# Performance work log

Hardware: AMD Instinct MI355X
Metric: run time of the kernel (lower is better)

The kernel has to match this reference:

```python
import jax, jax.numpy as jnp
import numpy as np

DIM = 1024
STATE = 256
B, S = 4, 4096

def setup_inputs() -> dict:
    key = jax.random.key(0)
    ks = jax.random.split(key, 8)
    sc_b = 1.0 / np.sqrt(DIM)
    sc_c = 1.0 / np.sqrt(STATE)
    return {
        "x": jax.random.normal(ks[0], (B, S, DIM), dtype=jnp.float32),
        "A": jax.random.normal(ks[1], (STATE,), dtype=jnp.float32) * 0.02,
        "B_w": jax.random.uniform(ks[2], (STATE, DIM), minval=-sc_b, maxval=sc_b),
        "B_b": jax.random.uniform(ks[3], (STATE,), minval=-sc_b, maxval=sc_b),
        "C_w": jax.random.uniform(ks[4], (DIM, STATE), minval=-sc_c, maxval=sc_c),
        "C_b": jax.random.uniform(ks[5], (DIM,), minval=-sc_c, maxval=sc_c),
        "D_w": jax.random.uniform(ks[6], (DIM, DIM), minval=-sc_b, maxval=sc_b),
        "D_b": jax.random.uniform(ks[7], (DIM,), minval=-sc_b, maxval=sc_b),
    }

def reference(x, A, B_w, B_b, C_w, C_b, D_w, D_b):
    # Precompute input projections in batch (the per-step loop only needs state*A + Bu)
    Bu = jnp.einsum('bsd,nd->bsn', x, B_w) + B_b          # [B,S,STATE]
    Du = jnp.einsum('bsd,ed->bse', x, D_w) + D_b          # [B,S,DIM]
    Aexp = jnp.exp(A)[None, :]                             # [1,STATE]
    state0 = jnp.zeros((x.shape[0], A.shape[0]), dtype=x.dtype)

    def step(state, bu_t):
        state = jnp.tanh(state * Aexp + bu_t)
        return state, state

    _, states = jax.lax.scan(step, state0, jnp.swapaxes(Bu, 0, 1))  # [S,B,STATE]
    states = jnp.swapaxes(states, 0, 1)                              # [B,S,STATE]
    y = jnp.einsum('bsn,en->bse', states, C_w) + C_b + Du
    return y
```

## Files before the change

### kernel.cpp

```cpp
#include <hip/hip_runtime.h>
#include <hip/hip_bf16.h>

#define DIM 1024
#define STATE 256
#define BATCH 4
#define SEQ 4096
#define M_TOT (BATCH * SEQ)

typedef short short8 __attribute__((ext_vector_type(8)));
typedef float f32x4 __attribute__((ext_vector_type(4)));

__device__ __forceinline__ unsigned short f2bf(float f) {
  unsigned int u = __float_as_uint(f);
  u += 0x7fff + ((u >> 16) & 1);
  return (unsigned short)(u >> 16);
}

__device__ __forceinline__ void gl_lds16(const void* g, void* l) {
  __builtin_amdgcn_global_load_lds(
      (const __attribute__((address_space(1))) void*)g,
      (__attribute__((address_space(3))) void*)l, 16, 0, 0);
}

#define C2F 2.8853900817779268f
#define LOG2EF 1.4426950408889634f
#define VMC(N) asm volatile("s_waitcnt vmcnt(" #N ")" ::: "memory")

__global__ __launch_bounds__(256) void convert_w(
    const float* __restrict__ A, const float* __restrict__ Bw,
    const float* __restrict__ Bb, const float* __restrict__ Cw,
    const float* __restrict__ Cb, const float* __restrict__ Dw,
    const float* __restrict__ Db, unsigned short* __restrict__ bwb,
    unsigned short* __restrict__ wob, float* __restrict__ bb2,
    float* __restrict__ mP2, float* __restrict__ cbdb) {
  const int bx = blockIdx.x;
  const int t = threadIdx.x;
  if (bx < 256) {
    int c = t * 4;
    const float4 v = *(const float4*)(Bw + (size_t)bx * DIM + c);
    *(ushort4*)(bwb + (size_t)bx * DIM + c) =
        make_ushort4(f2bf(v.x), f2bf(v.y), f2bf(v.z), f2bf(v.w));
  } else if (bx < 256 + 1024) {
    int e = bx - 256;
    if (t < 64) {
      const float4 v = *(const float4*)(Cw + (size_t)e * STATE + t * 4);
      *(ushort4*)(wob + (size_t)e * 1280 + t * 4) =
          make_ushort4(f2bf(v.x), f2bf(v.y), f2bf(v.z), f2bf(v.w));
    }
    const float4 v = *(const float4*)(Dw + (size_t)e * DIM + t * 4);
    *(ushort4*)(wob + (size_t)e * 1280 + 256 + t * 4) =
        make_ushort4(f2bf(v.x), f2bf(v.y), f2bf(v.z), f2bf(v.w));
  } else {
    const float P = C2F * __builtin_amdgcn_exp2f(A[t] * LOG2EF);
    bb2[t] = fmaf(Bb[t], C2F, P);
    mP2[t] = -2.0f * P;
#pragma unroll
    for (int k = 0; k < 4; ++k) {
      const int i = t * 4 + k;
      cbdb[i] = Cb[i] + Db[i];
    }
  }
}

__global__ __launch_bounds__(256, 2) void gemm_GX(
    const float* __restrict__ x,
    const unsigned short* __restrict__ bwb,
    float* __restrict__ G,
    const float* __restrict__ bb2,
    unsigned short* __restrict__ xb)
{
  __shared__ char lds[61440];

  const int tid = threadIdx.x;
  const int wave = tid >> 6;
  const int lane = tid & 63;
  const int lr = lane & 15;
  const int lk = lane >> 4;
  const int m0 = blockIdx.x * 32;

  f32x4 acc[2][4];
#pragma unroll
  for (int i = 0; i < 2; ++i)
#pragma unroll
    for (int j = 0; j < 4; ++j) acc[i][j] = (f32x4){0.f, 0.f, 0.f, 0.f};

  const char* xB  = (const char*)x;
  const char* bwB = (const char*)bwb;
  char* xbB = (char*)xb;

  auto stage = [&](int kt) {
    if (kt >= 32) return;
    char* slot = lds + (kt % 3) * 20480;
    {
      const int r = tid >> 3;
      const int c = (tid & 7) ^ (r & 7);
      gl_lds16(xB + (size_t)(m0 + r) * 4096 + (size_t)kt * 128 + c * 16,
               slot + wave * 1024);
    }
#pragma unroll
    for (int i = 0; i < 4; ++i) {
      const int s = i * 256 + tid;
      const int r = s >> 2;
      const int c = s & 3;
      gl_lds16(bwB + (size_t)r * 2048 + (size_t)kt * 64 + c * 16,
               slot + 4096 + i * 4096 + wave * 1024);
    }
  };

  stage(0); stage(1);
  VMC(5);
  __builtin_amdgcn_s_barrier();

  for (int t = 0; t < 32; ++t) {
    stage(t + 2);

    const char* As = lds + (t % 3) * 20480;
    const char* Bs = As + 4096;

    short8 af[2], bfr[4];
#pragma unroll
    for (int f = 0; f < 2; ++f) {
      const int row = f * 16 + lr;
      const int sw = row & 7;
      const f32x4 a0 = *(const f32x4*)(As + row * 128 + (((2 * lk)     ^ sw) << 4));
      const f32x4 a1 = *(const f32x4*)(As + row * 128 + (((2 * lk + 1) ^ sw) << 4));
      short8 v;
#pragma unroll
      for (int j = 0; j < 4; ++j) {
        v[j]     = (short)f2bf(a0[j]);
        v[4 + j] = (short)f2bf(a1[j]);
      }
      af[f] = v;
    }
#pragma unroll
    for (int fj = 0; fj < 4; ++fj) {
      const int rb = wave * 64 + fj * 16 + lr;
      bfr[fj] = *(const short8*)(Bs + rb * 64 + (lk << 4));
    }
#pragma unroll
    for (int f = 0; f < 2; ++f)
#pragma unroll
      for (int fj = 0; fj < 4; ++fj)
        acc[f][fj] = __builtin_amdgcn_mfma_f32_16x16x32_bf16(af[f], bfr[fj], acc[f][fj], 0, 0, 0);

    if (wave == 0) {
#pragma unroll
      for (int f = 0; f < 2; ++f) {
        const int row = f * 16 + lr;
        *(short8*)(xbB + (size_t)(m0 + row) * 2048 + (size_t)t * 64 + lk * 16) = af[f];
      }
      if (t < 30) { VMC(7); } else { VMC(0); }
    } else {
      if (t < 30) { VMC(5); } else { VMC(0); }
    }
    __builtin_amdgcn_s_barrier();
  }

#pragma unroll
  for (int f = 0; f < 2; ++f)
#pragma unroll
    for (int fj = 0; fj < 4; ++fj)
#pragma unroll
      for (int j = 0; j < 4; ++j) {
        const int rg = m0 + f * 16 + lk * 4 + j;
        const int cg = wave * 64 + fj * 16 + lr;
        G[(size_t)rg * STATE + cg] = fmaf(acc[f][fj][j], C2F, bb2[cg]);
      }
}

__global__ __launch_bounds__(256) void scan_kernel(
    const float* __restrict__ G, const float* __restrict__ mP2arr,
    unsigned short* __restrict__ states) {
  const int b = blockIdx.x >> 6;
  const int chunk = blockIdx.x & 63;
  const int n = threadIdx.x;
  const int t0 = chunk * 64;
  const int start = (t0 > 128) ? (t0 - 128) : 0;
  const int nw = t0 - start;
  const int total = nw + 64;

  const float* g = G + ((size_t)b * SEQ + start) * STATE + n;
  unsigned short* q = states + ((size_t)b * SEQ + start) * STATE + n;
  const float mP2 = mP2arr[n];

  float r = 0.5f;
  constexpr int CH = 16;
  float cur[CH], nxt[CH];
#pragma unroll
  for (int j = 0; j < CH; ++j) cur[j] = g[(size_t)j * STATE];

  const int NC = total / CH;
  for (int c = 0; c < NC; ++c) {
    if (c + 1 < NC) {
      const float* pn = g + (size_t)(c + 1) * CH * STATE;
#pragma unroll
      for (int j = 0; j < CH; ++j) nxt[j] = pn[(size_t)j * STATE];
    }
    if (c * CH >= nw) {
      unsigned short* qc = q + (size_t)c * CH * STATE;
#pragma unroll
      for (int j = 0; j < CH; ++j) {
        const float t = fmaf(mP2, r, cur[j]);
        const float e = __builtin_amdgcn_exp2f(t);
        r = __builtin_amdgcn_rcpf(1.0f + e);
        const float s = fmaf(-2.0f, r, 1.0f);
        qc[(size_t)j * STATE] = f2bf(s);
      }
    } else {
#pragma unroll
      for (int j = 0; j < CH; ++j) {
        const float t = fmaf(mP2, r, cur[j]);
        const float e = __builtin_amdgcn_exp2f(t);
        r = __builtin_amdgcn_rcpf(1.0f + e);
      }
    }
    if (c + 1 < NC) {
#pragma unroll
      for (int j = 0; j < CH; ++j) cur[j] = nxt[j];
    }
  }
}

#define PH(TILE, Q, STG, VMST)                                                 \
  do {                                                                         \
    const char* As = lds + ((TILE) & 1) * 32768;                               \
    const char* Bs = lds + 65536 + ((TILE) & 1) * 32768;                       \
    if ((Q) == 0) {                                                            \
      _Pragma("unroll") for (int fj = 0; fj < 4; ++fj) {                       \
        const int r = wn * 64 + fj * 16 + lr;                                  \
        _Pragma("unroll") for (int kk = 0; kk < 2; ++kk)                       \
          bfr[fj][kk] = *(const short8*)(Bs + r * 128 +                        \
                                         (((kk * 4 + lk) ^ (r & 7)) << 4));    \
      }                                                                        \
    }                                                                          \
    short8 af[2][2];                                                           \
    _Pragma("unroll") for (int fl = 0; fl < 2; ++fl) {                         \
      const int r = wm * 128 + (Q) * 32 + fl * 16 + lr;                        \
      _Pragma("unroll") for (int kk = 0; kk < 2; ++kk)                         \
        af[fl][kk] = *(const short8*)(As + r * 128 +                           \
                                      (((kk * 4 + lk) ^ (r & 7)) << 4));       \
    }                                                                          \
    STG;                                                                       \
    if ((Q) == 0) asm volatile("s_waitcnt lgkmcnt(8)" ::: "memory");           \
    __builtin_amdgcn_s_barrier();                                              \
    __builtin_amdgcn_s_setprio(1);                                             \
    _Pragma("unroll") for (int kk = 0; kk < 2; ++kk)                           \
      _Pragma("unroll") for (int fl = 0; fl < 2; ++fl)                         \
        _Pragma("unroll") for (int fj = 0; fj < 4; ++fj)                       \
          acc[(Q) * 2 + fl][fj] = __builtin_amdgcn_mfma_f32_16x16x32_bf16(     \
              af[fl][kk], bfr[fj][kk], acc[(Q) * 2 + fl][fj], 0, 0, 0);        \
    __builtin_amdgcn_s_setprio(0);                                             \
    VMST;                                                                      \
    __builtin_amdgcn_s_barrier();                                              \
  } while (0)

__global__ __launch_bounds__(512, 2) void gemm_out(
    const unsigned short* __restrict__ stb,
    const unsigned short* __restrict__ xb,
    const unsigned short* __restrict__ wob,
    const float* __restrict__ cbdb,
    float* __restrict__ dout)
{
  __shared__ char lds[131072];

  const int tid = threadIdx.x;
  const int wave = tid >> 6;
  const int lane = tid & 63;
  const int lr = lane & 15;
  const int lk = lane >> 4;
  const int wm = wave >> 2;
  const int wn = wave & 3;

  const int bs = ((blockIdx.x & 7) << 5) | (blockIdx.x >> 3);
  const int m0 = (bs >> 2) * 256;
  const int n0 = (bs & 3) * 256;

  const char* stbB = (const char*)stb;
  const char* xbB  = (const char*)xb;
  const char* wobB = (const char*)wob;

  f32x4 acc[8][4];
#pragma unroll
  for (int i = 0; i < 8; ++i)
#pragma unroll
    for (int j = 0; j < 4; ++j) acc[i][j] = (f32x4){0.f, 0.f, 0.f, 0.f};

  auto stageA = [&](int kt, int h) {
    if (kt >= 20) return;
    const char* base;
    size_t str;
    size_t colb;
    if (kt < 4) { base = stbB; str = 512;  colb = (size_t)kt * 128; }
    else        { base = xbB;  str = 2048; colb = (size_t)(kt - 4) * 128; }
    base += (size_t)m0 * str;
#pragma unroll
    for (int i2 = 0; i2 < 2; ++i2) {
      const int s = i2 * 512 + tid;
      const int r = s >> 3;
      const int cl = (s & 7) ^ (r & 7);
      gl_lds16(base + (size_t)(h * 128 + r) * str + colb + cl * 16,
               lds + ((kt & 1) * 32768) + h * 16384 + i2 * 8192 + wave * 1024);
    }
  };
  auto stageB = [&](int kt, int h) {
    if (kt >= 20) return;
#pragma unroll
    for (int i2 = 0; i2 < 2; ++i2) {
      const int s = i2 * 512 + tid;
      const int r = s >> 3;
      const int cl = (s & 7) ^ (r & 7);
      gl_lds16(wobB + (size_t)(n0 + h * 128 + r) * 2560 + (size_t)kt * 128 + cl * 16,
               lds + 65536 + ((kt & 1) * 32768) + h * 16384 + i2 * 8192 + wave * 1024);
    }
  };

  stageA(0, 0); stageA(0, 1);
  stageB(0, 0); stageB(0, 1);
  stageB(1, 0); stageB(1, 1);
  VMC(4);
  __builtin_amdgcn_s_barrier();

  short8 bfr[4][2];
  for (int i = 0; i < 10; ++i) {
    const int e = 2 * i, o = e + 1;
    PH(e, 0, stageA(o, 0), );
    PH(e, 1, stageA(o, 1), );
    PH(e, 2, stageB(e + 2, 0), );
    PH(e, 3, stageB(e + 2, 1), if (i == 9) { VMC(0); } else { VMC(4); });
    PH(o, 0, stageA(e + 2, 0), );
    PH(o, 1, stageA(e + 2, 1), );
    PH(o, 2, stageB(o + 2, 0), );
    PH(o, 3, stageB(o + 2, 1), VMC(4));
  }

#pragma unroll
  for (int fj = 0; fj < 4; ++fj) {
    const int col = n0 + wn * 64 + fj * 16 + lr;
    const float cb = cbdb[col];
#pragma unroll
    for (int m = 0; m < 8; ++m) {
      const int rowb = m0 + wm * 128 + m * 16 + lk * 4;
#pragma unroll
      for (int j = 0; j < 4; ++j)
        dout[(size_t)(rowb + j) * DIM + col] = acc[m][fj][j] + cb;
    }
  }
}

extern "C" void kernel_launch(void* const* d_in, const int* in_sizes, int n_in,
                              void* d_out, int out_size, void* d_ws, size_t ws_size,
                              hipStream_t stream) {
  const float* x  = (const float*)d_in[0];
  const float* A  = (const float*)d_in[1];
  const float* Bw = (const float*)d_in[2];
  const float* Bb = (const float*)d_in[3];
  const float* Cw = (const float*)d_in[4];
  const float* Cb = (const float*)d_in[5];
  const float* Dw = (const float*)d_in[6];
  const float* Db = (const float*)d_in[7];
  float* dout = (float*)d_out;

  char* ws = (char*)d_ws;
  unsigned short* xb   = (unsigned short*)(ws);
  unsigned short* bwb  = (unsigned short*)(ws + 33554432);
  unsigned short* wob  = (unsigned short*)(ws + 34078720);
  float*          G    = (float*)         (ws + 36700160);
  unsigned short* stb  = (unsigned short*)(ws + 53477376);
  float*          bb2  = (float*)         (ws + 61865984);
  float*          mP2  = (float*)         (ws + 61867008);
  float*          cbdb = (float*)         (ws + 61868032);

  convert_w<<<256 + 1024 + 1, 256, 0, stream>>>(
      A, Bw, Bb, Cw, Cb, Dw, Db, bwb, wob, bb2, mP2, cbdb);
  gemm_GX<<<512, 256, 0, stream>>>(x, bwb, G, bb2, xb);
  scan_kernel<<<BATCH * 64, 256, 0, stream>>>(G, mP2, stb);
  gemm_out<<<256, 512, 0, stream>>>(stb, xb, wob, cbdb, dout);
}
```

Baseline: 96.10 us.

## Deepen GX GEMM pipeline to four stages, swizzle B tile, rotate xb writes

Moves the gemm_GX LDS ring from three to four slots with a prefetch distance of three, so more global-to-LDS loads are in flight. The B-weight tile now uses an XOR-swizzled, row-pair layout to cut LDS bank conflicts on the fragment reads. The bf16 copy of x is written by a different wave each iteration instead of always wave 0, which evens out the vmcnt waits. Raising LDS to 80KB may drop the two-blocks-per-CU occupancy, and the vmcnt bookkeeping has to stay exactly right.

```diff
diff --git a/kernel.cpp b/kernel.cpp
--- a/kernel.cpp
+++ b/kernel.cpp
@@ -69,7 +69,7 @@
     const float* __restrict__ bb2,
     unsigned short* __restrict__ xb)
 {
-  __shared__ char lds[61440];
+  __shared__ char lds[81920];
 
   const int tid = threadIdx.x;
   const int wave = tid >> 6;
@@ -90,7 +90,7 @@
 
   auto stage = [&](int kt) {
     if (kt >= 32) return;
-    char* slot = lds + (kt % 3) * 20480;
+    char* slot = lds + (kt & 3) * 20480;
     {
       const int r = tid >> 3;
       const int c = (tid & 7) ^ (r & 7);
@@ -100,21 +100,24 @@
 #pragma unroll
     for (int i = 0; i < 4; ++i) {
       const int s = i * 256 + tid;
-      const int r = s >> 2;
-      const int c = s & 3;
-      gl_lds16(bwB + (size_t)r * 2048 + (size_t)kt * 64 + c * 16,
+      const int p = s >> 3;
+      const int cp = s & 7;
+      const int c = cp ^ (p & 7);
+      const int n = 2 * p + (c >> 2);
+      const int kc = c & 3;
+      gl_lds16(bwB + (size_t)n * 2048 + (size_t)kt * 64 + kc * 16,
                slot + 4096 + i * 4096 + wave * 1024);
     }
   };
 
-  stage(0); stage(1);
-  VMC(5);
+  stage(0); stage(1); stage(2);
+  VMC(10);
   __builtin_amdgcn_s_barrier();
 
   for (int t = 0; t < 32; ++t) {
-    stage(t + 2);
-
-    const char* As = lds + (t % 3) * 20480;
+    stage(t + 3);
+
+    const char* As = lds + (t & 3) * 20480;
     const char* Bs = As + 4096;
 
     short8 af[2], bfr[4];
@@ -134,8 +137,10 @@
     }
 #pragma unroll
     for (int fj = 0; fj < 4; ++fj) {
-      const int rb = wave * 64 + fj * 16 + lr;
-      bfr[fj] = *(const short8*)(Bs + rb * 64 + (lk << 4));
+      const int n = wave * 64 + fj * 16 + lr;
+      const int p = n >> 1;
+      const int cp = (((n & 1) * 4 + lk)) ^ (p & 7);
+      bfr[fj] = *(const short8*)(Bs + p * 128 + (cp << 4));
     }
 #pragma unroll
     for (int f = 0; f < 2; ++f)
@@ -143,17 +148,20 @@
       for (int fj = 0; fj < 4; ++fj)
         acc[f][fj] = __builtin_amdgcn_mfma_f32_16x16x32_bf16(af[f], bfr[fj], acc[f][fj], 0, 0, 0);
 
-    if (wave == 0) {
+    if (((t ^ wave) & 3) == 0) {
 #pragma unroll
       for (int f = 0; f < 2; ++f) {
         const int row = f * 16 + lr;
         *(short8*)(xbB + (size_t)(m0 + row) * 2048 + (size_t)t * 64 + lk * 16) = af[f];
       }
-      if (t < 30) { VMC(7); } else { VMC(0); }
-    } else {
-      if (t < 30) { VMC(5); } else { VMC(0); }
-    }
-    __builtin_amdgcn_s_barrier();
+    }
+
+    if (t < 31) {
+      if (t < 29)       { VMC(10); }
+      else if (t == 29) { VMC(5); }
+      else              { VMC(0); }
+      __builtin_amdgcn_s_barrier();
+    }
   }
 
 #pragma unroll
```

Measured after the change: 96.10 us. Within noise of the previous version (-0.0%).

## Double K-tile in GX GEMM, store G as bf16, spread xb writes across waves

Applied to the files above, without the earlier changes.

The GX GEMM now uses K-tiles of 256 elements with double buffering instead of 128-element K-tiles with triple buffering. This halves the number of loop iterations and barriers, at the cost of 80 KB of LDS and a full vmcnt(0) wait before each barrier. The intermediate G is stored as bf16 rather than fp32, halving its write traffic and the scan's read traffic but lowering the precision of the scan input. The bf16 copy of x is now written by a rotating wave each iteration rather than always wave 0, balancing the store work.

```diff
diff --git a/kernel.cpp b/kernel.cpp
--- a/kernel.cpp
+++ b/kernel.cpp
@@ -14,6 +14,10 @@
   unsigned int u = __float_as_uint(f);
   u += 0x7fff + ((u >> 16) & 1);
   return (unsigned short)(u >> 16);
+}
+
+__device__ __forceinline__ float bf2f(unsigned short u) {
+  return __uint_as_float((unsigned int)u << 16);
 }
 
 __device__ __forceinline__ void gl_lds16(const void* g, void* l) {
@@ -65,11 +69,11 @@
 __global__ __launch_bounds__(256, 2) void gemm_GX(
     const float* __restrict__ x,
     const unsigned short* __restrict__ bwb,
-    float* __restrict__ G,
+    unsigned short* __restrict__ G,
     const float* __restrict__ bb2,
     unsigned short* __restrict__ xb)
 {
-  __shared__ char lds[61440];
+  __shared__ char lds[81920];
 
   const int tid = threadIdx.x;
   const int wave = tid >> 6;
@@ -89,71 +93,85 @@
   char* xbB = (char*)xb;
 
   auto stage = [&](int kt) {
-    if (kt >= 32) return;
-    char* slot = lds + (kt % 3) * 20480;
-    {
-      const int r = tid >> 3;
-      const int c = (tid & 7) ^ (r & 7);
-      gl_lds16(xB + (size_t)(m0 + r) * 4096 + (size_t)kt * 128 + c * 16,
-               slot + wave * 1024);
-    }
-#pragma unroll
-    for (int i = 0; i < 4; ++i) {
+    if (kt >= 16) return;
+    char* slot = lds + (kt & 1) * 40960;
+#pragma unroll
+    for (int i = 0; i < 2; ++i) {
       const int s = i * 256 + tid;
-      const int r = s >> 2;
-      const int c = s & 3;
-      gl_lds16(bwB + (size_t)r * 2048 + (size_t)kt * 64 + c * 16,
-               slot + 4096 + i * 4096 + wave * 1024);
+      const int r = s >> 4;
+      const int c = (s & 15) ^ (r & 7);
+      gl_lds16(xB + (size_t)(m0 + r) * 4096 + (size_t)kt * 256 + c * 16,
+               slot + i * 4096 + wave * 1024);
+    }
+#pragma unroll
+    for (int i = 0; i < 8; ++i) {
+      const int s = i * 256 + tid;
+      const int r = s >> 3;
+      const int c = (s & 7) ^ (r & 7);
+      gl_lds16(bwB + (size_t)r * 2048 + (size_t)kt * 128 + c * 16,
+               slot + 8192 + i * 4096 + wave * 1024);
     }
   };
 
-  stage(0); stage(1);
-  VMC(5);
+  stage(0);
+  VMC(0);
   __builtin_amdgcn_s_barrier();
-
-  for (int t = 0; t < 32; ++t) {
-    stage(t + 2);
-
-    const char* As = lds + (t % 3) * 20480;
-    const char* Bs = As + 4096;
-
-    short8 af[2], bfr[4];
-#pragma unroll
-    for (int f = 0; f < 2; ++f) {
-      const int row = f * 16 + lr;
-      const int sw = row & 7;
-      const f32x4 a0 = *(const f32x4*)(As + row * 128 + (((2 * lk)     ^ sw) << 4));
-      const f32x4 a1 = *(const f32x4*)(As + row * 128 + (((2 * lk + 1) ^ sw) << 4));
-      short8 v;
-#pragma unroll
-      for (int j = 0; j < 4; ++j) {
-        v[j]     = (short)f2bf(a0[j]);
-        v[4 + j] = (short)f2bf(a1[j]);
-      }
-      af[f] = v;
-    }
-#pragma unroll
-    for (int fj = 0; fj < 4; ++fj) {
-      const int rb = wave * 64 + fj * 16 + lr;
-      bfr[fj] = *(const short8*)(Bs + rb * 64 + (lk << 4));
-    }
-#pragma unroll
-    for (int f = 0; f < 2; ++f)
-#pragma unroll
-      for (int fj = 0; fj < 4; ++fj)
-        acc[f][fj] = __builtin_amdgcn_mfma_f32_16x16x32_bf16(af[f], bfr[fj], acc[f][fj], 0, 0, 0);
-
-    if (wave == 0) {
+  stage(1);
+
+  for (int t = 0; t < 16; ++t) {
+    const char* As = lds + (t & 1) * 40960;
+    const char* Bs = As + 8192;
+
+    short8 af[2][2];
+#pragma unroll
+    for (int kk = 0; kk < 2; ++kk)
 #pragma unroll
       for (int f = 0; f < 2; ++f) {
         const int row = f * 16 + lr;
-        *(short8*)(xbB + (size_t)(m0 + row) * 2048 + (size_t)t * 64 + lk * 16) = af[f];
-      }
-      if (t < 30) { VMC(7); } else { VMC(0); }
-    } else {
-      if (t < 30) { VMC(5); } else { VMC(0); }
-    }
-    __builtin_amdgcn_s_barrier();
+        const int sw = row & 7;
+        const f32x4 a0 = *(const f32x4*)(As + row * 256 + (((kk * 8 + 2 * lk)     ^ sw) << 4));
+        const f32x4 a1 = *(const f32x4*)(As + row * 256 + (((kk * 8 + 2 * lk + 1) ^ sw) << 4));
+        short8 v;
+#pragma unroll
+        for (int j = 0; j < 4; ++j) {
+          v[j]     = (short)f2bf(a0[j]);
+          v[4 + j] = (short)f2bf(a1[j]);
+        }
+        af[kk][f] = v;
+      }
+    short8 bfr[2][4];
+#pragma unroll
+    for (int kk = 0; kk < 2; ++kk)
+#pragma unroll
+      for (int fj = 0; fj < 4; ++fj) {
+        const int n = wave * 64 + fj * 16 + lr;
+        bfr[kk][fj] = *(const short8*)(Bs + n * 128 + (((kk * 4 + lk) ^ (n & 7)) << 4));
+      }
+#pragma unroll
+    for (int kk = 0; kk < 2; ++kk)
+#pragma unroll
+      for (int f = 0; f < 2; ++f)
+#pragma unroll
+        for (int fj = 0; fj < 4; ++fj)
+          acc[f][fj] = __builtin_amdgcn_mfma_f32_16x16x32_bf16(
+              af[kk][f], bfr[kk][fj], acc[f][fj], 0, 0, 0);
+
+    if ((t & 3) == wave) {
+#pragma unroll
+      for (int kk = 0; kk < 2; ++kk)
+#pragma unroll
+        for (int f = 0; f < 2; ++f) {
+          const int row = f * 16 + lr;
+          *(short8*)(xbB + (size_t)(m0 + row) * 2048 +
+                     (size_t)t * 128 + kk * 64 + lk * 16) = af[kk][f];
+        }
+    }
+
+    if (t < 15) {
+      VMC(0);
+      __builtin_amdgcn_s_barrier();
+      stage(t + 2);
+    }
   }
 
 #pragma unroll
@@ -164,12 +182,12 @@
       for (int j = 0; j < 4; ++j) {
         const int rg = m0 + f * 16 + lk * 4 + j;
         const int cg = wave * 64 + fj * 16 + lr;
-        G[(size_t)rg * STATE + cg] = fmaf(acc[f][fj][j], C2F, bb2[cg]);
+        G[(size_t)rg * STATE + cg] = f2bf(fmaf(acc[f][fj][j], C2F, bb2[cg]));
       }
 }
 
 __global__ __launch_bounds__(256) void scan_kernel(
-    const float* __restrict__ G, const float* __restrict__ mP2arr,
+    const unsigned short* __restrict__ G, const float* __restrict__ mP2arr,
     unsigned short* __restrict__ states) {
   const int b = blockIdx.x >> 6;
   const int chunk = blockIdx.x & 63;
@@ -179,7 +197,7 @@
   const int nw = t0 - start;
   const int total = nw + 64;
 
-  const float* g = G + ((size_t)b * SEQ + start) * STATE + n;
+  const unsigned short* g = G + ((size_t)b * SEQ + start) * STATE + n;
   unsigned short* q = states + ((size_t)b * SEQ + start) * STATE + n;
   const float mP2 = mP2arr[n];
 
@@ -187,14 +205,14 @@
   constexpr int CH = 16;
   float cur[CH], nxt[CH];
 #pragma unroll
-  for (int j = 0; j < CH; ++j) cur[j] = g[(size_t)j * STATE];
+  for (int j = 0; j < CH; ++j) cur[j] = bf2f(g[(size_t)j * STATE]);
 
   const int NC = total / CH;
   for (int c = 0; c < NC; ++c) {
     if (c + 1 < NC) {
-      const float* pn = g + (size_t)(c + 1) * CH * STATE;
-#pragma unroll
-      for (int j = 0; j < CH; ++j) nxt[j] = pn[(size_t)j * STATE];
+      const unsigned short* pn = g + (size_t)(c + 1) * CH * STATE;
+#pragma unroll
+      for (int j = 0; j < CH; ++j) nxt[j] = bf2f(pn[(size_t)j * STATE]);
     }
     if (c * CH >= nw) {
       unsigned short* qc = q + (size_t)c * CH * STATE;
@@ -364,7 +382,7 @@
   unsigned short* xb   = (unsigned short*)(ws);
   unsigned short* bwb  = (unsigned short*)(ws + 33554432);
   unsigned short* wob  = (unsigned short*)(ws + 34078720);
-  float*          G    = (float*)         (ws + 36700160);
+  unsigned short* G    = (unsigned short*)(ws + 36700160);
   unsigned short* stb  = (unsigned short*)(ws + 53477376);
   float*          bb2  = (float*)         (ws + 61865984);
   float*          mP2  = (float*)         (ws + 61867008);
```

New measurement: 91.01 us. -5.3%, faster.
